# Kernel optimization log

Measured on AMD Instinct MI355X. Metric: run time of the kernel, lower is better.

The kernel has to match this reference:

```python
import jax, jax.numpy as jnp
import numpy as np

KERNELS = (9, 7, 5, 3)


def setup_inputs() -> dict:
    key = jax.random.key(0)
    ks = jax.random.split(key, 10)
    Nx = Ny = 512
    D = 256
    C = 8192
    H = 1024
    T = 5
    S = len(KERNELS)
    sc = 0.05
    node_emb = jax.random.normal(ks[0], (Nx * Ny, D), jnp.float32)
    tile_ids = jax.random.randint(ks[1], (C,), 0, Nx * Ny)
    cm = jax.random.randint(ks[2], (C, T), 0, 2, dtype=jnp.int32)
    create_mask = cm.at[:, 0].set(1)  # guarantee every city is eligible
    return dict(
        node_emb=node_emb,
        conv_W0=jax.random.normal(ks[3], (S, D, D), jnp.float32) * sc,
        conv_b0=jnp.zeros((S, D), jnp.float32),
        conv_W1=jax.random.normal(ks[4], (S, D, D), jnp.float32) * sc,
        conv_b1=jnp.zeros((S, D), jnp.float32),
        mlp_W0=jax.random.normal(ks[5], (D * (1 + S), H), jnp.float32) * sc,
        mlp_b0=jnp.zeros((H,), jnp.float32),
        mlp_W1=jax.random.normal(ks[6], (H, H), jnp.float32) * sc,
        mlp_b1=jnp.zeros((H,), jnp.float32),
        mlp_W2=jax.random.normal(ks[7], (H, T), jnp.float32) * sc,
        mlp_b2=jnp.zeros((T,), jnp.float32),
        tile_ids=tile_ids,
        create_mask=create_mask,
        Nx=Nx,
        Ny=Ny,
    )


def _forward(node_emb, conv_W0, conv_b0, conv_W1, conv_b1,
             mlp_W0, mlp_b0, mlp_W1, mlp_b1, mlp_W2, mlp_b2,
             tile_ids, create_mask, Nx, Ny):
    D = node_emb.shape[1]
    rmax = max(KERNELS) // 2
    # zero-padded spatial grid, matching F.unfold with padding=k//2
    grid = node_emb.reshape(Nx, Ny, D)
    padded = jnp.pad(grid, ((rmax, rmax), (rmax, rmax), (0, 0)))
    Wp = Ny + 2 * rmax
    pf = padded.reshape(-1, D)  # (padded_tiles, D)
    x = tile_ids // Ny
    y = tile_ids % Ny
    feats = [node_emb[tile_ids]]  # (C, D) raw city embedding
    for s, k in enumerate(KERNELS):
        r = k // 2
        off = jnp.arange(-r, r + 1)
        ix = x[:, None, None] + off[None, :, None] + rmax  # (C,k,1)
        iy = y[:, None, None] + off[None, None, :] + rmax  # (C,1,k)
        flat = ix * Wp + iy  # (C,k,k)
        pooled = pf[flat].mean(axis=(1, 2))  # (C,D) mean-pooled patch
        h = jax.nn.relu(pooled @ conv_W0[s] + conv_b0[s])
        h = h @ conv_W1[s] + conv_b1[s]  # n_conv_layers=2 projection
        feats.append(h)
    combined = jnp.concatenate(feats, axis=-1)  # (C, D*(1+S))
    h = jax.nn.relu(combined @ mlp_W0 + mlp_b0)
    h = jax.nn.relu(h @ mlp_W1 + mlp_b1)
    logits = h @ mlp_W2 + mlp_b2  # (C, T)
    mask = create_mask > 0
    # stable masked softmax
    neg_inf = jnp.array(-jnp.inf, logits.dtype)
    m = jnp.max(jnp.where(mask, logits, neg_inf), axis=-1, keepdims=True)
    e = jnp.where(mask, jnp.exp(logits - m), 0.0)
    probs = e / jnp.sum(e, axis=-1, keepdims=True)
    safe = jnp.clip(probs, 1e-8, None)
    entropies = -jnp.sum(probs * jnp.log(safe), axis=-1)
    logits_masked = jnp.where(mask, logits, neg_inf)
    return probs, entropies, logits_masked, mask


def reference(node_emb, conv_W0, conv_b0, conv_W1, conv_b1,
              mlp_W0, mlp_b0, mlp_W1, mlp_b1, mlp_W2, mlp_b2,
              tile_ids, create_mask, Nx, Ny):
    return _forward(node_emb, conv_W0, conv_b0, conv_W1, conv_b1,
                    mlp_W0, mlp_b0, mlp_W1, mlp_b1, mlp_W2, mlp_b2,
                    tile_ids, create_mask, Nx, Ny)
```

## Files before the change

### kernel.cpp

```cpp
#include <hip/hip_runtime.h>
#include <hip/hip_bf16.h>
#include <math.h>
#include <float.h>

#define NX 512
#define NY 512
#define DIM 256
#define CITIES 8192
#define HID 1024
#define TT 5
#define NS 4
#define COMB (DIM * (1 + NS))

typedef unsigned short u16;
typedef __attribute__((ext_vector_type(8))) short short8;
typedef __attribute__((ext_vector_type(8))) unsigned short ushort8;
typedef __attribute__((ext_vector_type(4))) unsigned short ushort4v;
typedef __attribute__((ext_vector_type(4))) float f32x4;

__device__ __forceinline__ u16 f2bf(float f) {
    __hip_bfloat16 h = __float2bfloat16(f);
    return __builtin_bit_cast(u16, h);
}
__device__ __forceinline__ float bf2f(u16 u) {
    __hip_bfloat16 h = __builtin_bit_cast(__hip_bfloat16, u);
    return __bfloat162float(h);
}

__global__ __launch_bounds__(256)
void prep_weights(const float* __restrict__ cW0, const float* __restrict__ cW1,
                  const float* __restrict__ mW0, const float* __restrict__ mW1,
                  u16* __restrict__ W0T, u16* __restrict__ W1T,
                  u16* __restrict__ Wm0T, u16* __restrict__ Wm1T) {
    __shared__ float tile[32][33];
    const int bid = blockIdx.x;
    const float* src;
    u16* dst;
    int K, N, bn, bk;
    if (bid < 512) {
        const float* s0 = (bid < 256) ? cW0 : cW1;
        u16* d0 = (bid < 256) ? W0T : W1T;
        int b = bid & 255;
        int batch = b >> 6;
        int t = b & 63;
        src = s0 + (size_t)batch * DIM * DIM;
        dst = d0 + (size_t)batch * DIM * DIM;
        K = DIM; N = DIM;
        bn = (t & 7) * 32;
        bk = (t >> 3) * 32;
    } else if (bid < 512 + 1280) {
        int b = bid - 512;
        src = mW0; dst = Wm0T; K = COMB; N = HID;
        bn = (b & 31) * 32;
        bk = (b >> 5) * 32;
    } else {
        int b = bid - 1792;
        src = mW1; dst = Wm1T; K = HID; N = HID;
        bn = (b & 31) * 32;
        bk = (b >> 5) * 32;
    }
    const int tx = threadIdx.x & 31, ty = threadIdx.x >> 5;
#pragma unroll
    for (int i = 0; i < 32; i += 8)
        tile[ty + i][tx] = src[(size_t)(bk + ty + i) * N + bn + tx];
    __syncthreads();
#pragma unroll
    for (int i = 0; i < 32; i += 8)
        dst[(size_t)(bn + ty + i) * K + bk + tx] = f2bf(tile[tx][ty + i]);
}

__global__ __launch_bounds__(256)
void pool_kernel(const float* __restrict__ node_emb,
                 const int* __restrict__ tile_ids,
                 u16* __restrict__ P,
                 u16* __restrict__ combined) {
    const int w    = threadIdx.x >> 6;
    const int lane = threadIdx.x & 63;
    const int c    = blockIdx.x * 4 + w;
    const int tile = tile_ids[c];
    const int x = tile >> 9;
    const int y = tile & 511;
    f32x4 s3 = {0,0,0,0}, s5 = {0,0,0,0}, s7 = {0,0,0,0}, s9 = {0,0,0,0};
    f32x4 ctr = {0,0,0,0};
#pragma unroll
    for (int dx = -4; dx <= 4; ++dx) {
        int gx = x + dx;
        bool okx = ((unsigned)gx < (unsigned)NX);
#pragma unroll
        for (int dy = -4; dy <= 4; ++dy) {
            int gy = y + dy;
            f32x4 v = {0,0,0,0};
            if (okx && ((unsigned)gy < (unsigned)NY)) {
                v = *((const f32x4*)&node_emb[(size_t)((gx << 9) + gy) * DIM]
                      + lane);
            }
            s9 += v;
            const int ax = dx < 0 ? -dx : dx;
            const int ay = dy < 0 ? -dy : dy;
            if (ax <= 3 && ay <= 3) s7 += v;
            if (ax <= 2 && ay <= 2) s5 += v;
            if (ax <= 1 && ay <= 1) s3 += v;
            if (dx == 0 && dy == 0) ctr = v;
        }
    }
    auto pack = [](f32x4 v) {
        ushort4v r;
        r.x = f2bf(v.x); r.y = f2bf(v.y); r.z = f2bf(v.z); r.w = f2bf(v.w);
        return r;
    };
    *(ushort4v*)&combined[(size_t)c * COMB + lane * 4] = pack(ctr);
    *(ushort4v*)&P[((size_t)c * NS + 0) * DIM + lane * 4] = pack(s9 * (1.f / 81.f));
    *(ushort4v*)&P[((size_t)c * NS + 1) * DIM + lane * 4] = pack(s7 * (1.f / 49.f));
    *(ushort4v*)&P[((size_t)c * NS + 2) * DIM + lane * 4] = pack(s5 * (1.f / 25.f));
    *(ushort4v*)&P[((size_t)c * NS + 3) * DIM + lane * 4] = pack(s3 * (1.f / 9.f));
}

__global__ __launch_bounds__(256)
void gemm_bf16(const u16* __restrict__ A, int lda, long aZ,
               const u16* __restrict__ BT, int ldb, long bZ,
               const float* __restrict__ bias, long biasZ,
               u16* __restrict__ C, int ldc, long cZ,
               int K, int relu) {
    __shared__ u16 ldsA[128 * 64];
    __shared__ u16 ldsB[128 * 64];
    A    += (size_t)blockIdx.z * aZ;
    BT   += (size_t)blockIdx.z * bZ;
    bias += (size_t)blockIdx.z * biasZ;
    C    += (size_t)blockIdx.z * cZ;

    int bx = blockIdx.x, by = blockIdx.y;
    {
        const int nwg = gridDim.x * gridDim.y;
        if ((nwg & 7) == 0) {
            const int bid = by * gridDim.x + bx;
            const int cpx = nwg >> 3;
            const int swz = (bid & 7) * cpx + (bid >> 3);
            bx = swz % gridDim.x;
            by = swz / gridDim.x;
        }
    }

    const int t    = threadIdx.x;
    const int lane = t & 63;
    const int wid  = t >> 6;
    const int wm   = wid >> 1;
    const int wn   = wid & 1;
    const int m0   = by * 128;
    const int n0   = bx * 128;

    const int srow0 = wid * 32 + (lane >> 3);
    const int c7    = lane & 7;
    const int fr    = lane & 15;
    const int kq    = lane >> 4;

    f32x4 acc[4][4];
#pragma unroll
    for (int m = 0; m < 4; ++m)
#pragma unroll
        for (int n = 0; n < 4; ++n) acc[m][n] = (f32x4){0.f, 0.f, 0.f, 0.f};

    for (int k0 = 0; k0 < K; k0 += 64) {
        __syncthreads();
#pragma unroll
        for (int i = 0; i < 4; ++i) {
            const int row = srow0 + i * 8;
            const int sc  = c7 ^ (row & 7);
            const u16* ga = A + (size_t)(m0 + row) * lda + k0 + sc * 8;
            __builtin_amdgcn_global_load_lds(
                (const __attribute__((address_space(1))) void*)ga,
                (__attribute__((address_space(3))) void*)(ldsA + (wid * 32 + i * 8) * 64),
                16, 0, 0);
        }
#pragma unroll
        for (int i = 0; i < 4; ++i) {
            const int row = srow0 + i * 8;
            const int sc  = c7 ^ (row & 7);
            const u16* gb = BT + (size_t)(n0 + row) * ldb + k0 + sc * 8;
            __builtin_amdgcn_global_load_lds(
                (const __attribute__((address_space(1))) void*)gb,
                (__attribute__((address_space(3))) void*)(ldsB + (wid * 32 + i * 8) * 64),
                16, 0, 0);
        }
        __syncthreads();

#pragma unroll
        for (int kk = 0; kk < 2; ++kk) {
            short8 af[4], bfr[4];
#pragma unroll
            for (int m = 0; m < 4; ++m) {
                const int r  = wm * 64 + m * 16 + fr;
                const int ck = (kk * 4 + kq) ^ (r & 7);
                af[m] = *(const short8*)(ldsA + r * 64 + ck * 8);
            }
#pragma unroll
            for (int n = 0; n < 4; ++n) {
                const int r  = wn * 64 + n * 16 + fr;
                const int ck = (kk * 4 + kq) ^ (r & 7);
                bfr[n] = *(const short8*)(ldsB + r * 64 + ck * 8);
            }
#pragma unroll
            for (int m = 0; m < 4; ++m)
#pragma unroll
                for (int n = 0; n < 4; ++n)
                    acc[m][n] = __builtin_amdgcn_mfma_f32_16x16x32_bf16(
                        af[m], bfr[n], acc[m][n], 0, 0, 0);
        }
    }

#pragma unroll
    for (int n = 0; n < 4; ++n) {
        const int col = n0 + wn * 64 + n * 16 + fr;
        const float bv = bias[col];
#pragma unroll
        for (int m = 0; m < 4; ++m) {
            const int row = m0 + wm * 64 + m * 16 + kq * 4;
#pragma unroll
            for (int r = 0; r < 4; ++r) {
                float v = acc[m][n][r] + bv;
                if (relu) v = fmaxf(v, 0.f);
                C[(size_t)(row + r) * ldc + col] = f2bf(v);
            }
        }
    }
}

__global__ __launch_bounds__(256)
void head_kernel(const u16* __restrict__ g2,
                 const float* __restrict__ W2,
                 const float* __restrict__ b2,
                 const int* __restrict__ create_mask,
                 float* __restrict__ out) {
    const int w    = threadIdx.x >> 6;
    const int lane = threadIdx.x & 63;
    const int c    = blockIdx.x * 4 + w;
    const u16* gr = g2 + (size_t)c * HID + lane * 16;
    ushort8 v0 = *(const ushort8*)(gr);
    ushort8 v1 = *(const ushort8*)(gr + 8);
    float acc[TT] = {0.f, 0.f, 0.f, 0.f, 0.f};
    const int kbase = lane * 16;
#pragma unroll
    for (int e = 0; e < 8; ++e) {
        float g = bf2f(v0[e]);
#pragma unroll
        for (int tt = 0; tt < TT; ++tt) acc[tt] += g * W2[(kbase + e) * TT + tt];
    }
#pragma unroll
    for (int e = 0; e < 8; ++e) {
        float g = bf2f(v1[e]);
#pragma unroll
        for (int tt = 0; tt < TT; ++tt) acc[tt] += g * W2[(kbase + 8 + e) * TT + tt];
    }
#pragma unroll
    for (int off = 32; off > 0; off >>= 1) {
#pragma unroll
        for (int tt = 0; tt < TT; ++tt)
            acc[tt] += __shfl_down(acc[tt], off, 64);
    }
    if (lane == 0) {
        float l[TT];
        int mk[TT];
#pragma unroll
        for (int tt = 0; tt < TT; ++tt) {
            l[tt]  = acc[tt] + b2[tt];
            mk[tt] = create_mask[(size_t)c * TT + tt];
        }
        float m = -INFINITY;
#pragma unroll
        for (int tt = 0; tt < TT; ++tt)
            if (mk[tt]) m = fmaxf(m, l[tt]);
        float e[TT];
        float s = 0.f;
#pragma unroll
        for (int tt = 0; tt < TT; ++tt) {
            e[tt] = mk[tt] ? expf(l[tt] - m) : 0.f;
            s += e[tt];
        }
        float inv = 1.f / s;
        float ent = 0.f;
        float* probs   = out;
        float* entrop  = out + (size_t)5 * CITIES;
        float* lmasked = out + (size_t)6 * CITIES;
        float* maskout = out + (size_t)11 * CITIES;
#pragma unroll
        for (int tt = 0; tt < TT; ++tt) {
            float p = e[tt] * inv;
            probs[(size_t)c * TT + tt] = p;
            ent -= p * logf(fmaxf(p, 1e-8f));
            lmasked[(size_t)c * TT + tt] = mk[tt] ? l[tt] : -1e30f;
            maskout[(size_t)c * TT + tt] = mk[tt] ? 1.f : 0.f;
        }
        entrop[c] = ent;
    }
}

extern "C" void kernel_launch(void* const* d_in, const int* in_sizes, int n_in,
                              void* d_out, int out_size, void* d_ws, size_t ws_size,
                              hipStream_t stream) {
    const float* node_emb = (const float*)d_in[0];
    const float* conv_W0  = (const float*)d_in[1];
    const float* conv_b0  = (const float*)d_in[2];
    const float* conv_W1  = (const float*)d_in[3];
    const float* conv_b1  = (const float*)d_in[4];
    const float* mlp_W0   = (const float*)d_in[5];
    const float* mlp_b0   = (const float*)d_in[6];
    const float* mlp_W1   = (const float*)d_in[7];
    const float* mlp_b1   = (const float*)d_in[8];
    const float* mlp_W2   = (const float*)d_in[9];
    const float* mlp_b2   = (const float*)d_in[10];
    const int*   tile_ids = (const int*)d_in[11];
    const int*   cmask    = (const int*)d_in[12];
    float* out = (float*)d_out;

    char* w = (char*)d_ws;
    u16* P_bf   = (u16*)w;                    w += (size_t)CITIES * NS * DIM * 2;
    u16* comb   = (u16*)w;                    w += (size_t)CITIES * COMB * 2;
    u16* h0     = (u16*)w;                    w += (size_t)CITIES * NS * DIM * 2;
    u16* g1     = (u16*)w;                    w += (size_t)CITIES * HID * 2;
    u16* g2     = (u16*)w;                    w += (size_t)CITIES * HID * 2;
    u16* W0T    = (u16*)w;                    w += (size_t)NS * DIM * DIM * 2;
    u16* W1T    = (u16*)w;                    w += (size_t)NS * DIM * DIM * 2;
    u16* Wm0T   = (u16*)w;                    w += (size_t)HID * COMB * 2;
    u16* Wm1T   = (u16*)w;                    w += (size_t)HID * HID * 2;

    prep_weights<<<2816, 256, 0, stream>>>(conv_W0, conv_W1, mlp_W0, mlp_W1,
                                           W0T, W1T, Wm0T, Wm1T);

    pool_kernel<<<CITIES / 4, 256, 0, stream>>>(node_emb, tile_ids, P_bf, comb);

    gemm_bf16<<<dim3(DIM/128, CITIES/128, NS), 256, 0, stream>>>(
        P_bf, NS * DIM, DIM,
        W0T, DIM, (long)DIM * DIM,
        conv_b0, DIM,
        h0, NS * DIM, DIM,
        DIM, 1);
    gemm_bf16<<<dim3(DIM/128, CITIES/128, NS), 256, 0, stream>>>(
        h0, NS * DIM, DIM,
        W1T, DIM, (long)DIM * DIM,
        conv_b1, DIM,
        comb + DIM, COMB, DIM,
        DIM, 0);

    gemm_bf16<<<dim3(HID/128, CITIES/128, 1), 256, 0, stream>>>(
        comb, COMB, 0,
        Wm0T, COMB, 0,
        mlp_b0, 0,
        g1, HID, 0,
        COMB, 1);
    gemm_bf16<<<dim3(HID/128, CITIES/128, 1), 256, 0, stream>>>(
        g1, HID, 0,
        Wm1T, HID, 0,
        mlp_b1, 0,
        g2, HID, 0,
        HID, 1);

    head_kernel<<<CITIES / 4, 256, 0, stream>>>(g2, mlp_W2, mlp_b2, cmask, out);
}
```

Before: 531.5 us.

## Fuse conv GEMM pair with LDS-resident hidden, merge prep and pool kernels

Merges the weight transpose/convert kernel and the pooling kernel into a single launch that dispatches on block index. Replaces the two per-scale conv GEMM launches with one kernel that computes relu(P·W0+b0) into a 64KB LDS tile and then multiplies it by W1, writing straight into the combined buffer. This drops the h0 round-trip through global memory and two launches. The cost is a large LDS footprint (~96KB per 512-thread block), which lowers occupancy, and column-strided scalar bf16 stores into comb.

```diff
diff --git a/kernel.cpp b/kernel.cpp
--- a/kernel.cpp
+++ b/kernel.cpp
@@ -28,55 +28,55 @@
 }
 
 __global__ __launch_bounds__(256)
-void prep_weights(const float* __restrict__ cW0, const float* __restrict__ cW1,
-                  const float* __restrict__ mW0, const float* __restrict__ mW1,
-                  u16* __restrict__ W0T, u16* __restrict__ W1T,
-                  u16* __restrict__ Wm0T, u16* __restrict__ Wm1T) {
-    __shared__ float tile[32][33];
+void prep_pool(const float* __restrict__ cW0, const float* __restrict__ cW1,
+               const float* __restrict__ mW0, const float* __restrict__ mW1,
+               u16* __restrict__ W0T, u16* __restrict__ W1T,
+               u16* __restrict__ Wm0T, u16* __restrict__ Wm1T,
+               const float* __restrict__ node_emb,
+               const int* __restrict__ tile_ids,
+               u16* __restrict__ P,
+               u16* __restrict__ combined) {
     const int bid = blockIdx.x;
-    const float* src;
-    u16* dst;
-    int K, N, bn, bk;
-    if (bid < 512) {
-        const float* s0 = (bid < 256) ? cW0 : cW1;
-        u16* d0 = (bid < 256) ? W0T : W1T;
-        int b = bid & 255;
-        int batch = b >> 6;
-        int t = b & 63;
-        src = s0 + (size_t)batch * DIM * DIM;
-        dst = d0 + (size_t)batch * DIM * DIM;
-        K = DIM; N = DIM;
-        bn = (t & 7) * 32;
-        bk = (t >> 3) * 32;
-    } else if (bid < 512 + 1280) {
-        int b = bid - 512;
-        src = mW0; dst = Wm0T; K = COMB; N = HID;
-        bn = (b & 31) * 32;
-        bk = (b >> 5) * 32;
-    } else {
-        int b = bid - 1792;
-        src = mW1; dst = Wm1T; K = HID; N = HID;
-        bn = (b & 31) * 32;
-        bk = (b >> 5) * 32;
-    }
-    const int tx = threadIdx.x & 31, ty = threadIdx.x >> 5;
-#pragma unroll
-    for (int i = 0; i < 32; i += 8)
-        tile[ty + i][tx] = src[(size_t)(bk + ty + i) * N + bn + tx];
-    __syncthreads();
-#pragma unroll
-    for (int i = 0; i < 32; i += 8)
-        dst[(size_t)(bn + ty + i) * K + bk + tx] = f2bf(tile[tx][ty + i]);
-}
-
-__global__ __launch_bounds__(256)
-void pool_kernel(const float* __restrict__ node_emb,
-                 const int* __restrict__ tile_ids,
-                 u16* __restrict__ P,
-                 u16* __restrict__ combined) {
+    if (bid < 2816) {
+        __shared__ float tile[32][33];
+        const float* src;
+        u16* dst;
+        int K, N, bn, bk;
+        if (bid < 512) {
+            const float* s0 = (bid < 256) ? cW0 : cW1;
+            u16* d0 = (bid < 256) ? W0T : W1T;
+            int b = bid & 255;
+            int batch = b >> 6;
+            int t = b & 63;
+            src = s0 + (size_t)batch * DIM * DIM;
+            dst = d0 + (size_t)batch * DIM * DIM;
+            K = DIM; N = DIM;
+            bn = (t & 7) * 32;
+            bk = (t >> 3) * 32;
+        } else if (bid < 512 + 1280) {
+            int b = bid - 512;
+            src = mW0; dst = Wm0T; K = COMB; N = HID;
+            bn = (b & 31) * 32;
+            bk = (b >> 5) * 32;
+        } else {
+            int b = bid - 1792;
+            src = mW1; dst = Wm1T; K = HID; N = HID;
+            bn = (b & 31) * 32;
+            bk = (b >> 5) * 32;
+        }
+        const int tx = threadIdx.x & 31, ty = threadIdx.x >> 5;
+#pragma unroll
+        for (int i = 0; i < 32; i += 8)
+            tile[ty + i][tx] = src[(size_t)(bk + ty + i) * N + bn + tx];
+        __syncthreads();
+#pragma unroll
+        for (int i = 0; i < 32; i += 8)
+            dst[(size_t)(bn + ty + i) * K + bk + tx] = f2bf(tile[tx][ty + i]);
+        return;
+    }
     const int w    = threadIdx.x >> 6;
     const int lane = threadIdx.x & 63;
-    const int c    = blockIdx.x * 4 + w;
+    const int c    = (bid - 2816) * 4 + w;
     const int tile = tile_ids[c];
     const int x = tile >> 9;
     const int y = tile & 511;
@@ -113,6 +113,161 @@
     *(ushort4v*)&P[((size_t)c * NS + 1) * DIM + lane * 4] = pack(s7 * (1.f / 49.f));
     *(ushort4v*)&P[((size_t)c * NS + 2) * DIM + lane * 4] = pack(s5 * (1.f / 25.f));
     *(ushort4v*)&P[((size_t)c * NS + 3) * DIM + lane * 4] = pack(s3 * (1.f / 9.f));
+}
+
+__global__ __launch_bounds__(512)
+void conv_fused(const u16* __restrict__ P,
+                const u16* __restrict__ W0T,
+                const u16* __restrict__ W1T,
+                const float* __restrict__ b0,
+                const float* __restrict__ b1,
+                u16* __restrict__ comb) {
+    __shared__ u16 ldsA[128 * 64];
+    __shared__ u16 ldsB[256 * 64];
+    __shared__ u16 ldsH[128 * 256];
+
+    const int s    = blockIdx.y;
+    const int m0   = blockIdx.x * 128;
+    const int lane = threadIdx.x & 63;
+    const int wid  = threadIdx.x >> 6;
+    const int wr   = wid >> 2;
+    const int wc   = wid & 3;
+    const int fr   = lane & 15;
+    const int kq   = lane >> 4;
+    const int l8   = lane >> 3;
+    const int c7   = lane & 7;
+
+    const u16* A  = P + (size_t)s * DIM;
+    const u16* B0 = W0T + (size_t)s * DIM * DIM;
+    const u16* B1 = W1T + (size_t)s * DIM * DIM;
+    const float* bias0 = b0 + s * DIM;
+    const float* bias1 = b1 + s * DIM;
+
+    f32x4 acc[4][4];
+#pragma unroll
+    for (int m = 0; m < 4; ++m)
+#pragma unroll
+        for (int n = 0; n < 4; ++n) acc[m][n] = (f32x4){0.f, 0.f, 0.f, 0.f};
+
+    for (int k0 = 0; k0 < DIM; k0 += 64) {
+        __syncthreads();
+#pragma unroll
+        for (int i = 0; i < 2; ++i) {
+            const int row = wid * 16 + i * 8 + l8;
+            const int sc  = c7 ^ (row & 7);
+            const u16* ga = A + (size_t)(m0 + row) * (NS * DIM) + k0 + sc * 8;
+            __builtin_amdgcn_global_load_lds(
+                (const __attribute__((address_space(1))) void*)ga,
+                (__attribute__((address_space(3))) void*)(ldsA + (wid * 16 + i * 8) * 64),
+                16, 0, 0);
+        }
+#pragma unroll
+        for (int i = 0; i < 4; ++i) {
+            const int row = wid * 32 + i * 8 + l8;
+            const int sc  = c7 ^ (row & 7);
+            const u16* gb = B0 + (size_t)row * DIM + k0 + sc * 8;
+            __builtin_amdgcn_global_load_lds(
+                (const __attribute__((address_space(1))) void*)gb,
+                (__attribute__((address_space(3))) void*)(ldsB + (wid * 32 + i * 8) * 64),
+                16, 0, 0);
+        }
+        __syncthreads();
+#pragma unroll
+        for (int kk = 0; kk < 2; ++kk) {
+            short8 af[4], bf[4];
+#pragma unroll
+            for (int m = 0; m < 4; ++m) {
+                const int r  = wr * 64 + m * 16 + fr;
+                const int ck = (kk * 4 + kq) ^ (r & 7);
+                af[m] = *(const short8*)(ldsA + r * 64 + ck * 8);
+            }
+#pragma unroll
+            for (int n = 0; n < 4; ++n) {
+                const int r  = wc * 64 + n * 16 + fr;
+                const int ck = (kk * 4 + kq) ^ (r & 7);
+                bf[n] = *(const short8*)(ldsB + r * 64 + ck * 8);
+            }
+#pragma unroll
+            for (int m = 0; m < 4; ++m)
+#pragma unroll
+                for (int n = 0; n < 4; ++n)
+                    acc[m][n] = __builtin_amdgcn_mfma_f32_16x16x32_bf16(
+                        af[m], bf[n], acc[m][n], 0, 0, 0);
+        }
+    }
+
+#pragma unroll
+    for (int n = 0; n < 4; ++n) {
+        const int col = wc * 64 + n * 16 + fr;
+        const float bv = bias0[col];
+#pragma unroll
+        for (int m = 0; m < 4; ++m) {
+            const int rbase = wr * 64 + m * 16 + kq * 4;
+#pragma unroll
+            for (int r = 0; r < 4; ++r) {
+                const int row = rbase + r;
+                const float v = fmaxf(acc[m][n][r] + bv, 0.f);
+                ldsH[row * 256 + (((col >> 3) ^ (row & 7)) * 8) + (col & 7)] = f2bf(v);
+            }
+        }
+    }
+#pragma unroll
+    for (int m = 0; m < 4; ++m)
+#pragma unroll
+        for (int n = 0; n < 4; ++n) acc[m][n] = (f32x4){0.f, 0.f, 0.f, 0.f};
+    __syncthreads();
+
+    for (int k0 = 0; k0 < DIM; k0 += 64) {
+        __syncthreads();
+#pragma unroll
+        for (int i = 0; i < 4; ++i) {
+            const int row = wid * 32 + i * 8 + l8;
+            const int sc  = c7 ^ (row & 7);
+            const u16* gb = B1 + (size_t)row * DIM + k0 + sc * 8;
+            __builtin_amdgcn_global_load_lds(
+                (const __attribute__((address_space(1))) void*)gb,
+                (__attribute__((address_space(3))) void*)(ldsB + (wid * 32 + i * 8) * 64),
+                16, 0, 0);
+        }
+        __syncthreads();
+#pragma unroll
+        for (int kk = 0; kk < 2; ++kk) {
+            short8 af[4], bf[4];
+#pragma unroll
+            for (int m = 0; m < 4; ++m) {
+                const int r  = wr * 64 + m * 16 + fr;
+                const int ch = (k0 >> 3) + kk * 4 + kq;
+                const int ph = ch ^ (r & 7);
+                af[m] = *(const short8*)(ldsH + r * 256 + ph * 8);
+            }
+#pragma unroll
+            for (int n = 0; n < 4; ++n) {
+                const int r  = wc * 64 + n * 16 + fr;
+                const int ck = (kk * 4 + kq) ^ (r & 7);
+                bf[n] = *(const short8*)(ldsB + r * 64 + ck * 8);
+            }
+#pragma unroll
+            for (int m = 0; m < 4; ++m)
+#pragma unroll
+                for (int n = 0; n < 4; ++n)
+                    acc[m][n] = __builtin_amdgcn_mfma_f32_16x16x32_bf16(
+                        af[m], bf[n], acc[m][n], 0, 0, 0);
+        }
+    }
+
+#pragma unroll
+    for (int n = 0; n < 4; ++n) {
+        const int col = wc * 64 + n * 16 + fr;
+        const int cg  = DIM * (1 + s) + col;
+        const float bv = bias1[col];
+#pragma unroll
+        for (int m = 0; m < 4; ++m) {
+            const int rowb = m0 + wr * 64 + m * 16 + kq * 4;
+#pragma unroll
+            for (int r = 0; r < 4; ++r)
+                comb[(size_t)(rowb + r) * COMB + cg] = f2bf(acc[m][n][r] + bv);
+        }
+    }
 }
 
 __global__ __launch_bounds__(256)
@@ -314,7 +469,6 @@
     char* w = (char*)d_ws;
     u16* P_bf   = (u16*)w;                    w += (size_t)CITIES * NS * DIM * 2;
     u16* comb   = (u16*)w;                    w += (size_t)CITIES * COMB * 2;
-    u16* h0     = (u16*)w;                    w += (size_t)CITIES * NS * DIM * 2;
     u16* g1     = (u16*)w;                    w += (size_t)CITIES * HID * 2;
     u16* g2     = (u16*)w;                    w += (size_t)CITIES * HID * 2;
     u16* W0T    = (u16*)w;                    w += (size_t)NS * DIM * DIM * 2;
@@ -322,31 +476,21 @@
     u16* Wm0T   = (u16*)w;                    w += (size_t)HID * COMB * 2;
     u16* Wm1T   = (u16*)w;                    w += (size_t)HID * HID * 2;
 
-    prep_weights<<<2816, 256, 0, stream>>>(conv_W0, conv_W1, mlp_W0, mlp_W1,
-                                           W0T, W1T, Wm0T, Wm1T);
-
-    pool_kernel<<<CITIES / 4, 256, 0, stream>>>(node_emb, tile_ids, P_bf, comb);
-
-    gemm_bf16<<<dim3(DIM/128, CITIES/128, NS), 256, 0, stream>>>(
-        P_bf, NS * DIM, DIM,
-        W0T, DIM, (long)DIM * DIM,
-        conv_b0, DIM,
-        h0, NS * DIM, DIM,
-        DIM, 1);
-    gemm_bf16<<<dim3(DIM/128, CITIES/128, NS), 256, 0, stream>>>(
-        h0, NS * DIM, DIM,
-        W1T, DIM, (long)DIM * DIM,
-        conv_b1, DIM,
-        comb + DIM, COMB, DIM,
-        DIM, 0);
-
-    gemm_bf16<<<dim3(HID/128, CITIES/128, 1), 256, 0, stream>>>(
+    prep_pool<<<2816 + CITIES / 4, 256, 0, stream>>>(
+        conv_W0, conv_W1, mlp_W0, mlp_W1,
+        W0T, W1T, Wm0T, Wm1T,
+        node_emb, tile_ids, P_bf, comb);
+
+    conv_fused<<<dim3(CITIES / 128, NS), 512, 0, stream>>>(
+        P_bf, W0T, W1T, conv_b0, conv_b1, comb);
+
+    gemm_bf16<<<dim3(HID / 128, CITIES / 128, 1), 256, 0, stream>>>(
         comb, COMB, 0,
         Wm0T, COMB, 0,
         mlp_b0, 0,
         g1, HID, 0,
         COMB, 1);
-    gemm_bf16<<<dim3(HID/128, CITIES/128, 1), 256, 0, stream>>>(
+    gemm_bf16<<<dim3(HID / 128, CITIES / 128, 1), 256, 0, stream>>>(
         g1, HID, 0,
         Wm1T, HID, 0,
         mlp_b1, 0,
```

Result: no change. 529.4 us (-0.4%).
